# Optimization experiments

Measured on AMD Instinct MI355X. Metric: run time of the kernel, lower is better.

Reference implementation:

```python
import jax, jax.numpy as jnp
import numpy as np

B, H, S, D = 4, 16, 2048, 64
TEMPERATURE = 8.0  # sqrt(D)
NEG = -1000000000.0

def setup_inputs() -> dict:
    key = jax.random.key(0)
    kq, kk, kv, km = jax.random.split(key, 4)
    q = jax.random.normal(kq, (B, H, S, D), dtype=jnp.float32)
    k = jax.random.normal(kk, (B, H, S, D), dtype=jnp.float32)
    v = jax.random.normal(kv, (B, H, S, D), dtype=jnp.float32)
    mask = jax.random.randint(km, (B, 1, S, S), 0, 2, dtype=jnp.int32)
    return {"q": q, "k": k, "v": v, "mask": mask}

def reference(q, k, v, mask):
    # scores: [B,H,S,S]
    scores = jnp.einsum('bhqd,bhkd->bhqk', q / TEMPERATURE, k)
    scores = jnp.where(mask == 1, NEG, scores)
    attn = jax.nn.softmax(scores, axis=-1)  # dropout p=0.0 -> identity
    out = jnp.einsum('bhqk,bhkd->bhqd', attn, v)
    return out
```

## Files before the change

kernel.cpp:

```cpp
#include <hip/hip_runtime.h>

#define NB 4
#define NH 16
#define SS 2048
#define DD 64
#define QT 128
#define KT 32
#define KSP 72
#define VSP 40
#define QSCALE 0.18033688011112042f
#define MASK_BITS_BYTES ((size_t)NB * SS * (SS / 8))

typedef __bf16 bf16x8 __attribute__((ext_vector_type(8)));
typedef __bf16 bf16x2 __attribute__((ext_vector_type(2)));
typedef float  floatx16 __attribute__((ext_vector_type(16)));

static_assert(sizeof(bf16x8) == 16, "bf16x8 must be 16B");

__device__ __forceinline__ int pack2(float a, float b) {
    bf16x2 v; v[0] = (__bf16)a; v[1] = (__bf16)b;
    return __builtin_bit_cast(int, v);
}

__global__ __launch_bounds__(256)
void pack_mask_kernel(const int* __restrict__ M, unsigned long long* __restrict__ bits)
{
    int gw   = (blockIdx.x * 256 + threadIdx.x) >> 6;
    int lane = threadIdx.x & 63;
    size_t row = (size_t)(gw >> 5);
    int word   = gw & 31;
    int mval = M[row * SS + (size_t)word * 64 + lane];
    unsigned long long b = __ballot(mval == 1);
    if (lane == 0) bits[gw] = b;
}

template<bool USE_BITS>
__global__ __launch_bounds__(256, 4)
void attn_kernel(const float* __restrict__ Q, const float* __restrict__ K,
                 const float* __restrict__ V, const int* __restrict__ M,
                 const unsigned* __restrict__ MB, float* __restrict__ O)
{
    __shared__ __bf16 ks[KT][KSP];
    __shared__ __bf16 vsT[DD][VSP];

    const int t    = threadIdx.x;
    const int wave = t >> 6;
    const int lane = t & 63;
    const int l31  = lane & 31;
    const int h8   = lane >> 5;

    const int bh    = blockIdx.x >> 4;
    const int qtile = blockIdx.x & 15;
    const int b     = bh >> 4;
    const int q0    = qtile * QT + wave * 32;

    const size_t base = (size_t)bh * SS * DD;
    const float* Qb = Q + base;
    const float* Kb = K + base;
    const float* Vb = V + base;

    bf16x8 aq[4];
    {
        const float* qp = Qb + (size_t)(q0 + l31) * DD + 8 * h8;
        #pragma unroll
        for (int s = 0; s < 4; ++s) {
            float4 f0 = *(const float4*)(qp + 16 * s);
            float4 f1 = *(const float4*)(qp + 16 * s + 4);
            bf16x8 a;
            a[0] = (__bf16)(f0.x * QSCALE); a[1] = (__bf16)(f0.y * QSCALE);
            a[2] = (__bf16)(f0.z * QSCALE); a[3] = (__bf16)(f0.w * QSCALE);
            a[4] = (__bf16)(f1.x * QSCALE); a[5] = (__bf16)(f1.y * QSCALE);
            a[6] = (__bf16)(f1.z * QSCALE); a[7] = (__bf16)(f1.w * QSCALE);
            aq[s] = a;
        }
    }

    const int skey = t >> 3;
    const int sdc  = (t & 7) * 8;
    const int vk   = 2 * (t & 15);
    const int vdc  = (t >> 4) * 4;
    const int vcol = 16 * (vk >> 4) + 8 * ((vk >> 2) & 1) + (vk & 3) + 4 * ((vk >> 3) & 1);

    const float* kp0 = Kb + (size_t)skey * DD + sdc;
    const float* vp0 = Vb + (size_t)vk * DD + vdc;

    float4 ka0 = ((const float4*)kp0)[0];
    float4 ka1 = ((const float4*)kp0)[1];
    float4 va0 = *(const float4*)vp0;
    float4 va1 = *(const float4*)(vp0 + DD);

    const unsigned* mbrow = MB + ((size_t)b * SS + q0 + l31) * (SS / 32);
    const int*      mrow  = M + (size_t)b * SS * SS + (size_t)(q0 + l31) * SS + 4 * h8;

    floatx16 o0, o1;
    #pragma unroll
    for (int i = 0; i < 16; ++i) { o0[i] = 0.f; o1[i] = 0.f; }
    float ls = 0.f;

    for (int tt = 0; tt < SS / KT; ++tt) {
        __syncthreads();

        {
            bf16x8 kw;
            kw[0]=(__bf16)ka0.x; kw[1]=(__bf16)ka0.y; kw[2]=(__bf16)ka0.z; kw[3]=(__bf16)ka0.w;
            kw[4]=(__bf16)ka1.x; kw[5]=(__bf16)ka1.y; kw[6]=(__bf16)ka1.z; kw[7]=(__bf16)ka1.w;
            *(bf16x8*)&ks[skey][sdc] = kw;
            float av[4] = {va0.x, va0.y, va0.z, va0.w};
            float bv[4] = {va1.x, va1.y, va1.z, va1.w};
            #pragma unroll
            for (int i = 0; i < 4; ++i) {
                bf16x2 pr; pr[0] = (__bf16)av[i]; pr[1] = (__bf16)bv[i];
                *(bf16x2*)&vsT[vdc + i][vcol] = pr;
            }
        }
        __syncthreads();

        unsigned mw = 0;
        int4 mi[4];
        if (USE_BITS) {
            mw = mbrow[tt];
        } else {
            #pragma unroll
            for (int g2 = 0; g2 < 4; ++g2)
                mi[g2] = *(const int4*)(mrow + tt * KT + 8 * g2);
        }

        {
            int jn = ((tt + 1) * KT) & (SS - 1);
            const float* kn = kp0 + (size_t)jn * DD;
            ka0 = ((const float4*)kn)[0];
            ka1 = ((const float4*)kn)[1];
            const float* vn = vp0 + (size_t)jn * DD;
            va0 = *(const float4*)vn;
            va1 = *(const float4*)(vn + DD);
        }

        floatx16 c;
        #pragma unroll
        for (int i = 0; i < 16; ++i) c[i] = 0.f;
        #pragma unroll
        for (int s = 0; s < 4; ++s) {
            bf16x8 a = *(const bf16x8*)&ks[l31][16 * s + 8 * h8];
            c = __builtin_amdgcn_mfma_f32_32x32x16_bf16(a, aq[s], c, 0, 0, 0);
        }

        unsigned u = mw >> (4 * h8);
        int pk[8];
        float psum = 0.f;
        #pragma unroll
        for (int g = 0; g < 8; ++g) {
            const int ia = 2 * g, ib = 2 * g + 1;
            float pa = __builtin_amdgcn_exp2f(c[ia]);
            float pb = __builtin_amdgcn_exp2f(c[ib]);
            bool ma, mb_;
            if (USE_BITS) {
                ma  = (u >> ((ia & 3) + 8 * (ia >> 2))) & 1;
                mb_ = (u >> ((ib & 3) + 8 * (ib >> 2))) & 1;
            } else {
                const int g2 = ia >> 2;
                ma  = ((&mi[g2].x)[ia & 3] == 1);
                mb_ = ((&mi[g2].x)[ib & 3] == 1);
            }
            pa = ma  ? 0.f : pa;
            pb = mb_ ? 0.f : pb;
            psum += pa + pb;
            pk[g] = pack2(pa, pb);
        }
        ls += psum;

        #pragma unroll
        for (int s2 = 0; s2 < 2; ++s2) {
            int4 fw; fw.x = pk[4*s2]; fw.y = pk[4*s2+1]; fw.z = pk[4*s2+2]; fw.w = pk[4*s2+3];
            bf16x8 bp = __builtin_bit_cast(bf16x8, fw);
            bf16x8 av0 = *(const bf16x8*)&vsT[l31][16 * s2 + 8 * h8];
            bf16x8 av1 = *(const bf16x8*)&vsT[32 + l31][16 * s2 + 8 * h8];
            o0 = __builtin_amdgcn_mfma_f32_32x32x16_bf16(av0, bp, o0, 0, 0, 0);
            o1 = __builtin_amdgcn_mfma_f32_32x32x16_bf16(av1, bp, o1, 0, 0, 0);
        }
    }

    ls += __shfl_xor(ls, 32);
    float inv = 1.0f / ls;
    float* op = O + base + (size_t)(q0 + l31) * DD;
    #pragma unroll
    for (int s = 0; s < 4; ++s) {
        float4 st0, st1;
        st0.x = o0[4*s+0] * inv; st0.y = o0[4*s+1] * inv;
        st0.z = o0[4*s+2] * inv; st0.w = o0[4*s+3] * inv;
        st1.x = o1[4*s+0] * inv; st1.y = o1[4*s+1] * inv;
        st1.z = o1[4*s+2] * inv; st1.w = o1[4*s+3] * inv;
        *(float4*)(op + 8 * s + 4 * h8)      = st0;
        *(float4*)(op + 32 + 8 * s + 4 * h8) = st1;
    }
}

extern "C" void kernel_launch(void* const* d_in, const int* in_sizes, int n_in,
                              void* d_out, int out_size, void* d_ws, size_t ws_size,
                              hipStream_t stream) {
    (void)in_sizes; (void)n_in; (void)out_size;
    const float* q = (const float*)d_in[0];
    const float* k = (const float*)d_in[1];
    const float* v = (const float*)d_in[2];
    const int*   m = (const int*)d_in[3];
    float* out = (float*)d_out;
    dim3 grid(NB * NH * (SS / QT));

    if (ws_size >= MASK_BITS_BYTES) {
        unsigned long long* bits = (unsigned long long*)d_ws;
        pack_mask_kernel<<<dim3(NB * SS * (SS / 64) / 4), 256, 0, stream>>>(m, bits);
        attn_kernel<true><<<grid, 256, 0, stream>>>(q, k, v, m, (const unsigned*)bits, out);
    } else {
        attn_kernel<false><<<grid, 256, 0, stream>>>(q, k, v, m, (const unsigned*)nullptr, out);
    }
}
```

Baseline: 309.4 us.

## Double-buffer 64-key tiles, reorder grid, add setprio, grid-stride mask packing

Doubles the key tile to 64 and double-buffers the K/V shared-memory tiles, which drops one barrier per iteration. The mask bits are now read as a single 64-bit word per tile. The grid order is changed so that consecutive blocks cover different batch-heads, and s_setprio is raised around the MFMA sections. The mask-packing kernel becomes grid-stride with fewer blocks. These changes target barrier overhead, per-iteration loop cost and launch overhead, at the price of more registers and LDS, which may lower occupancy.

```diff
diff --git a/kernel.cpp b/kernel.cpp
--- a/kernel.cpp
+++ b/kernel.cpp
@@ -5,15 +5,17 @@
 #define SS 2048
 #define DD 64
 #define QT 128
-#define KT 32
+#define KT 64
+#define NT (SS / KT)
 #define KSP 72
-#define VSP 40
+#define VSP 72
 #define QSCALE 0.18033688011112042f
 #define MASK_BITS_BYTES ((size_t)NB * SS * (SS / 8))
 
 typedef __bf16 bf16x8 __attribute__((ext_vector_type(8)));
 typedef __bf16 bf16x2 __attribute__((ext_vector_type(2)));
 typedef float  floatx16 __attribute__((ext_vector_type(16)));
+typedef unsigned long long u64t;
 
 static_assert(sizeof(bf16x8) == 16, "bf16x8 must be 16B");
 
@@ -23,15 +25,19 @@
 }
 
 __global__ __launch_bounds__(256)
-void pack_mask_kernel(const int* __restrict__ M, unsigned long long* __restrict__ bits)
+void pack_mask_kernel(const int* __restrict__ M, u64t* __restrict__ bits)
 {
-    int gw   = (blockIdx.x * 256 + threadIdx.x) >> 6;
-    int lane = threadIdx.x & 63;
-    size_t row = (size_t)(gw >> 5);
-    int word   = gw & 31;
-    int mval = M[row * SS + (size_t)word * 64 + lane];
-    unsigned long long b = __ballot(mval == 1);
-    if (lane == 0) bits[gw] = b;
+    const int w    = (blockIdx.x * 256 + threadIdx.x) >> 6;
+    const int lane = threadIdx.x & 63;
+    #pragma unroll 4
+    for (int i = 0; i < 32; ++i) {
+        const int gw   = i * 8192 + w;
+        const size_t row = (size_t)(gw >> 5);
+        const int word = gw & 31;
+        const int mval = M[row * SS + (size_t)word * 64 + lane];
+        const u64t b = __ballot(mval == 1);
+        if (lane == 0) bits[gw] = b;
+    }
 }
 
 template<bool USE_BITS>
@@ -40,8 +46,8 @@
                  const float* __restrict__ V, const int* __restrict__ M,
                  const unsigned* __restrict__ MB, float* __restrict__ O)
 {
-    __shared__ __bf16 ks[KT][KSP];
-    __shared__ __bf16 vsT[DD][VSP];
+    __shared__ __bf16 ks [2][KT][KSP];
+    __shared__ __bf16 vsT[2][DD][VSP];
 
     const int t    = threadIdx.x;
     const int wave = t >> 6;
@@ -49,8 +55,8 @@
     const int l31  = lane & 31;
     const int h8   = lane >> 5;
 
-    const int bh    = blockIdx.x >> 4;
-    const int qtile = blockIdx.x & 15;
+    const int bh    = blockIdx.x & 63;
+    const int qtile = blockIdx.x >> 6;
     const int b     = bh >> 4;
     const int q0    = qtile * QT + wave * 32;
 
@@ -86,96 +92,116 @@
 
     float4 ka0 = ((const float4*)kp0)[0];
     float4 ka1 = ((const float4*)kp0)[1];
-    float4 va0 = *(const float4*)vp0;
+    float4 kb0 = ((const float4*)(kp0 + 32 * DD))[0];
+    float4 kb1 = ((const float4*)(kp0 + 32 * DD))[1];
+    float4 va0 = *(const float4*)(vp0);
     float4 va1 = *(const float4*)(vp0 + DD);
-
-    const unsigned* mbrow = MB + ((size_t)b * SS + q0 + l31) * (SS / 32);
-    const int*      mrow  = M + (size_t)b * SS * SS + (size_t)(q0 + l31) * SS + 4 * h8;
+    float4 vb0 = *(const float4*)(vp0 + 32 * DD);
+    float4 vb1 = *(const float4*)(vp0 + 33 * DD);
+
+    const u64t* mbrow = (const u64t*)MB + ((size_t)b * SS + q0 + l31) * (SS / 64);
+    const int*  mrow  = M + (size_t)b * SS * SS + (size_t)(q0 + l31) * SS + 4 * h8;
 
     floatx16 o0, o1;
     #pragma unroll
     for (int i = 0; i < 16; ++i) { o0[i] = 0.f; o1[i] = 0.f; }
     float ls = 0.f;
 
-    for (int tt = 0; tt < SS / KT; ++tt) {
-        __syncthreads();
+    for (int tt = 0; tt < NT; ++tt) {
+        const int cur = tt & 1;
 
         {
             bf16x8 kw;
             kw[0]=(__bf16)ka0.x; kw[1]=(__bf16)ka0.y; kw[2]=(__bf16)ka0.z; kw[3]=(__bf16)ka0.w;
             kw[4]=(__bf16)ka1.x; kw[5]=(__bf16)ka1.y; kw[6]=(__bf16)ka1.z; kw[7]=(__bf16)ka1.w;
-            *(bf16x8*)&ks[skey][sdc] = kw;
-            float av[4] = {va0.x, va0.y, va0.z, va0.w};
-            float bv[4] = {va1.x, va1.y, va1.z, va1.w};
+            *(bf16x8*)&ks[cur][skey][sdc] = kw;
+            kw[0]=(__bf16)kb0.x; kw[1]=(__bf16)kb0.y; kw[2]=(__bf16)kb0.z; kw[3]=(__bf16)kb0.w;
+            kw[4]=(__bf16)kb1.x; kw[5]=(__bf16)kb1.y; kw[6]=(__bf16)kb1.z; kw[7]=(__bf16)kb1.w;
+            *(bf16x8*)&ks[cur][skey + 32][sdc] = kw;
             #pragma unroll
             for (int i = 0; i < 4; ++i) {
-                bf16x2 pr; pr[0] = (__bf16)av[i]; pr[1] = (__bf16)bv[i];
-                *(bf16x2*)&vsT[vdc + i][vcol] = pr;
+                bf16x2 pr;
+                pr[0] = (__bf16)(&va0.x)[i]; pr[1] = (__bf16)(&va1.x)[i];
+                *(bf16x2*)&vsT[cur][vdc + i][vcol] = pr;
+                pr[0] = (__bf16)(&vb0.x)[i]; pr[1] = (__bf16)(&vb1.x)[i];
+                *(bf16x2*)&vsT[cur][vdc + i][32 + vcol] = pr;
             }
         }
         __syncthreads();
 
-        unsigned mw = 0;
-        int4 mi[4];
+        u64t mall = 0;
+        int4 mi[8];
         if (USE_BITS) {
-            mw = mbrow[tt];
+            mall = mbrow[tt];
         } else {
             #pragma unroll
-            for (int g2 = 0; g2 < 4; ++g2)
-                mi[g2] = *(const int4*)(mrow + tt * KT + 8 * g2);
+            for (int g = 0; g < 8; ++g)
+                mi[g] = *(const int4*)(mrow + tt * KT + 8 * g);
         }
 
         {
-            int jn = ((tt + 1) * KT) & (SS - 1);
+            const int jn = ((tt + 1) * KT) & (SS - 1);
             const float* kn = kp0 + (size_t)jn * DD;
             ka0 = ((const float4*)kn)[0];
             ka1 = ((const float4*)kn)[1];
+            kb0 = ((const float4*)(kn + 32 * DD))[0];
+            kb1 = ((const float4*)(kn + 32 * DD))[1];
             const float* vn = vp0 + (size_t)jn * DD;
-            va0 = *(const float4*)vn;
+            va0 = *(const float4*)(vn);
             va1 = *(const float4*)(vn + DD);
-        }
-
-        floatx16 c;
+            vb0 = *(const float4*)(vn + 32 * DD);
+            vb1 = *(const float4*)(vn + 33 * DD);
+        }
+
         #pragma unroll
-        for (int i = 0; i < 16; ++i) c[i] = 0.f;
-        #pragma unroll
-        for (int s = 0; s < 4; ++s) {
-            bf16x8 a = *(const bf16x8*)&ks[l31][16 * s + 8 * h8];
-            c = __builtin_amdgcn_mfma_f32_32x32x16_bf16(a, aq[s], c, 0, 0, 0);
-        }
-
-        unsigned u = mw >> (4 * h8);
-        int pk[8];
-        float psum = 0.f;
-        #pragma unroll
-        for (int g = 0; g < 8; ++g) {
-            const int ia = 2 * g, ib = 2 * g + 1;
-            float pa = __builtin_amdgcn_exp2f(c[ia]);
-            float pb = __builtin_amdgcn_exp2f(c[ib]);
-            bool ma, mb_;
-            if (USE_BITS) {
-                ma  = (u >> ((ia & 3) + 8 * (ia >> 2))) & 1;
-                mb_ = (u >> ((ib & 3) + 8 * (ib >> 2))) & 1;
-            } else {
-                const int g2 = ia >> 2;
-                ma  = ((&mi[g2].x)[ia & 3] == 1);
-                mb_ = ((&mi[g2].x)[ib & 3] == 1);
-            }
-            pa = ma  ? 0.f : pa;
-            pb = mb_ ? 0.f : pb;
-            psum += pa + pb;
-            pk[g] = pack2(pa, pb);
-        }
-        ls += psum;
-
-        #pragma unroll
-        for (int s2 = 0; s2 < 2; ++s2) {
-            int4 fw; fw.x = pk[4*s2]; fw.y = pk[4*s2+1]; fw.z = pk[4*s2+2]; fw.w = pk[4*s2+3];
-            bf16x8 bp = __builtin_bit_cast(bf16x8, fw);
-            bf16x8 av0 = *(const bf16x8*)&vsT[l31][16 * s2 + 8 * h8];
-            bf16x8 av1 = *(const bf16x8*)&vsT[32 + l31][16 * s2 + 8 * h8];
-            o0 = __builtin_amdgcn_mfma_f32_32x32x16_bf16(av0, bp, o0, 0, 0, 0);
-            o1 = __builtin_amdgcn_mfma_f32_32x32x16_bf16(av1, bp, o1, 0, 0, 0);
+        for (int half = 0; half < 2; ++half) {
+            floatx16 c;
+            #pragma unroll
+            for (int i = 0; i < 16; ++i) c[i] = 0.f;
+            __builtin_amdgcn_s_setprio(1);
+            #pragma unroll
+            for (int s = 0; s < 4; ++s) {
+                bf16x8 a = *(const bf16x8*)&ks[cur][32 * half + l31][16 * s + 8 * h8];
+                c = __builtin_amdgcn_mfma_f32_32x32x16_bf16(a, aq[s], c, 0, 0, 0);
+            }
+            __builtin_amdgcn_s_setprio(0);
+
+            const unsigned mw = USE_BITS ? (unsigned)(mall >> (32 * half)) : 0u;
+            const unsigned u  = mw >> (4 * h8);
+            int pk[8];
+            float psum = 0.f;
+            #pragma unroll
+            for (int g = 0; g < 8; ++g) {
+                const int ia = 2 * g, ib = 2 * g + 1;
+                float pa = __builtin_amdgcn_exp2f(c[ia]);
+                float pb = __builtin_amdgcn_exp2f(c[ib]);
+                bool ma, mb_;
+                if (USE_BITS) {
+                    ma  = (u >> ((ia & 3) + 8 * (ia >> 2))) & 1;
+                    mb_ = (u >> ((ib & 3) + 8 * (ib >> 2))) & 1;
+                } else {
+                    const int g2 = 4 * half + (ia >> 2);
+                    ma  = ((&mi[g2].x)[ia & 3] == 1);
+                    mb_ = ((&mi[g2].x)[ib & 3] == 1);
+                }
+                pa = ma  ? 0.f : pa;
+                pb = mb_ ? 0.f : pb;
+                psum += pa + pb;
+                pk[g] = pack2(pa, pb);
+            }
+            ls += psum;
+
+            __builtin_amdgcn_s_setprio(1);
+            #pragma unroll
+            for (int s2 = 0; s2 < 2; ++s2) {
+                int4 fw; fw.x = pk[4*s2]; fw.y = pk[4*s2+1]; fw.z = pk[4*s2+2]; fw.w = pk[4*s2+3];
+                bf16x8 bp = __builtin_bit_cast(bf16x8, fw);
+                bf16x8 av0 = *(const bf16x8*)&vsT[cur][l31][32 * half + 16 * s2 + 8 * h8];
+                bf16x8 av1 = *(const bf16x8*)&vsT[cur][32 + l31][32 * half + 16 * s2 + 8 * h8];
+                o0 = __builtin_amdgcn_mfma_f32_32x32x16_bf16(av0, bp, o0, 0, 0, 0);
+                o1 = __builtin_amdgcn_mfma_f32_32x32x16_bf16(av1, bp, o1, 0, 0, 0);
+            }
+            __builtin_amdgcn_s_setprio(0);
         }
     }
 
@@ -206,8 +232,8 @@
     dim3 grid(NB * NH * (SS / QT));
 
     if (ws_size >= MASK_BITS_BYTES) {
-        unsigned long long* bits = (unsigned long long*)d_ws;
-        pack_mask_kernel<<<dim3(NB * SS * (SS / 64) / 4), 256, 0, stream>>>(m, bits);
+        u64t* bits = (u64t*)d_ws;
+        pack_mask_kernel<<<dim3(2048), 256, 0, stream>>>(m, bits);
         attn_kernel<true><<<grid, 256, 0, stream>>>(q, k, v, m, (const unsigned*)bits, out);
     } else {
         attn_kernel<false><<<grid, 256, 0, stream>>>(q, k, v, m, (const unsigned*)nullptr, out);
```

New measurement: 281.0 us. -9.2%, faster.
